# Optimization experiments

Hardware: AMD Instinct MI355X
Metric: run time of the kernel (lower is better)

## Reference

```python
import jax, jax.numpy as jnp
import numpy as np

B, S, C, H, EPS = 8, 1024, 768, 12, 1e-6
D = C // H            # head dim 64
F_HID = int(C * 4.0)  # 3072


def _layer_norm(x, w, b):
    mu = jnp.mean(x, axis=-1, keepdims=True)
    var = jnp.mean(jnp.square(x - mu), axis=-1, keepdims=True)
    return (x - mu) * jax.lax.rsqrt(var + EPS) * w + b


def setup_inputs() -> dict:
    key = jax.random.key(0)
    ks = jax.random.split(key, 16)
    sc_c = 1.0 / np.sqrt(C)
    sc_f = 1.0 / np.sqrt(F_HID)
    return {
        "hidden_states": jax.random.normal(ks[0], (B, S, C), jnp.float32),
        "ln1_w": jnp.ones((C,), jnp.float32),
        "ln1_b": jnp.zeros((C,), jnp.float32),
        # weights stored [in, out] (transpose of torch Linear layout; same math)
        "q_w": jax.random.normal(ks[1], (C, C), jnp.float32) * sc_c,
        "q_b": jnp.zeros((C,), jnp.float32),
        "k_w": jax.random.normal(ks[2], (C, C), jnp.float32) * sc_c,
        "k_b": jnp.zeros((C,), jnp.float32),
        "v_w": jax.random.normal(ks[3], (C, C), jnp.float32) * sc_c,
        "v_b": jnp.zeros((C,), jnp.float32),
        "o_w": jax.random.normal(ks[4], (C, C), jnp.float32) * sc_c,
        "o_b": jnp.zeros((C,), jnp.float32),
        "lam1": jnp.ones((C,), jnp.float32),
        "ln2_w": jnp.ones((C,), jnp.float32),
        "ln2_b": jnp.zeros((C,), jnp.float32),
        "fc1_w": jax.random.normal(ks[5], (C, F_HID), jnp.float32) * sc_c,
        "fc1_b": jnp.zeros((F_HID,), jnp.float32),
        "fc2_w": jax.random.normal(ks[6], (F_HID, C), jnp.float32) * sc_f,
        "fc2_b": jnp.zeros((C,), jnp.float32),
    }


def reference(hidden_states, ln1_w, ln1_b, q_w, q_b, k_w, k_b, v_w, v_b,
              o_w, o_b, lam1, ln2_w, ln2_b, fc1_w, fc1_b, fc2_w, fc2_b):
    shortcut = hidden_states
    x = _layer_norm(hidden_states, ln1_w, ln1_b)
    # QKV projections, split heads: [B,S,C] -> [B,H,S,D]
    def heads(t):
        return t.reshape(B, S, H, D).transpose(0, 2, 1, 3)
    q = heads(x @ q_w + q_b)
    k = heads(x @ k_w + k_b)
    v = heads(x @ v_w + v_b)
    scores = jnp.einsum("bhsd,bhtd->bhst", q, k) / np.sqrt(D)
    probs = jax.nn.softmax(scores, axis=-1)  # dropout p=0 -> identity
    ctx = jnp.einsum("bhst,bhtd->bhsd", probs, v)
    ctx = ctx.transpose(0, 2, 1, 3).reshape(B, S, C)
    attn_out = ctx @ o_w + o_b
    hidden = attn_out * lam1 + shortcut
    y = _layer_norm(hidden, ln2_w, ln2_b)
    y = jax.nn.gelu(y @ fc1_w + fc1_b, approximate=False)
    y = y @ fc2_w + fc2_b
    return y * lam2_mul(lam1) + hidden if False else (y * jnp.ones_like(lam1) * lam1 * 0 + y) * 0 + y * lam1 * 0 + (y * _LAM2 + hidden)


# NOTE: layer_scale2 has its own parameter; expose it cleanly instead of the hack above.
_LAM2 = None

def lam2_mul(x):
    return x

# Clean final definitions (override the above):

def setup_inputs() -> dict:  # noqa: F811
    key = jax.random.key(0)
    ks = jax.random.split(key, 16)
    sc_c = 1.0 / np.sqrt(C)
    sc_f = 1.0 / np.sqrt(F_HID)
    return {
        "hidden_states": jax.random.normal(ks[0], (B, S, C), jnp.float32),
        "ln1_w": jnp.ones((C,), jnp.float32),
        "ln1_b": jnp.zeros((C,), jnp.float32),
        "q_w": jax.random.normal(ks[1], (C, C), jnp.float32) * sc_c,
        "q_b": jnp.zeros((C,), jnp.float32),
        "k_w": jax.random.normal(ks[2], (C, C), jnp.float32) * sc_c,
        "k_b": jnp.zeros((C,), jnp.float32),
        "v_w": jax.random.normal(ks[3], (C, C), jnp.float32) * sc_c,
        "v_b": jnp.zeros((C,), jnp.float32),
        "o_w": jax.random.normal(ks[4], (C, C), jnp.float32) * sc_c,
        "o_b": jnp.zeros((C,), jnp.float32),
        "lam1": jnp.ones((C,), jnp.float32),
        "ln2_w": jnp.ones((C,), jnp.float32),
        "ln2_b": jnp.zeros((C,), jnp.float32),
        "fc1_w": jax.random.normal(ks[5], (C, F_HID), jnp.float32) * sc_c,
        "fc1_b": jnp.zeros((F_HID,), jnp.float32),
        "fc2_w": jax.random.normal(ks[6], (F_HID, C), jnp.float32) * sc_f,
        "fc2_b": jnp.zeros((C,), jnp.float32),
        "lam2": jnp.ones((C,), jnp.float32),
    }


def reference(hidden_states, ln1_w, ln1_b, q_w, q_b, k_w, k_b, v_w, v_b,  # noqa: F811
              o_w, o_b, lam1, ln2_w, ln2_b, fc1_w, fc1_b, fc2_w, fc2_b, lam2):
    shortcut = hidden_states
    x = _layer_norm(hidden_states, ln1_w, ln1_b)
    def heads(t):
        return t.reshape(B, S, H, D).transpose(0, 2, 1, 3)  # [B,H,S,D]
    q = heads(x @ q_w + q_b)
    k = heads(x @ k_w + k_b)
    v = heads(x @ v_w + v_b)
    scores = jnp.einsum("bhsd,bhtd->bhst", q, k) / np.sqrt(D)
    probs = jax.nn.softmax(scores, axis=-1)  # attn dropout p=0 (eval)
    ctx = jnp.einsum("bhst,bhtd->bhsd", probs, v)
    ctx = ctx.transpose(0, 2, 1, 3).reshape(B, S, C)
    attn_out = ctx @ o_w + o_b            # SelfOutput dense (dropout p=0)
    hidden = attn_out * lam1 + shortcut   # layer_scale1 + residual
    y = _layer_norm(hidden, ln2_w, ln2_b)
    y = jax.nn.gelu(y @ fc1_w + fc1_b, approximate=False)  # nn.GELU exact
    y = y @ fc2_w + fc2_b
    return y * lam2 + hidden              # layer_scale2 + residual
```

## Files before the change

kernel.cpp:

```cpp
#include <hip/hip_runtime.h>
#include <hip/hip_bf16.h>
#include <stdint.h>
#include <stddef.h>

using bf16x8 = __attribute__((ext_vector_type(8))) short;
using f32x4  = __attribute__((ext_vector_type(4))) float;
using f32x16 = __attribute__((ext_vector_type(16))) float;

#define DEV static __device__ __forceinline__

DEV unsigned short f2bf(float f) {
  union { float f; uint32_t u; } x; x.f = f;
  uint32_t u = x.u;
  u += 0x7fffu + ((u >> 16) & 1u);
  return (unsigned short)(u >> 16);
}

DEV uint32_t pkbf(float a, float b) {
  __hip_bfloat162 t = __float22bfloat162_rn(float2{a, b});
  union { __hip_bfloat162 h; uint32_t u; } c; c.h = t; return c.u;
}

DEV void gld_lds16(const void* g, void* lds) {
  __builtin_amdgcn_global_load_lds(
      (__attribute__((address_space(1))) void*)(uintptr_t)g,
      (__attribute__((address_space(3))) void*)(uintptr_t)lds, 16, 0, 0);
}

__global__ void transpose_w(const float* __restrict__ in, unsigned short* __restrict__ out,
                            int K, int N) {
  __shared__ float tile[64][65];
  int n0 = blockIdx.x * 64, k0 = blockIdx.y * 64;
  int tx = threadIdx.x & 15, ty = threadIdx.x >> 4;
#pragma unroll
  for (int j = 0; j < 4; ++j) {
    int r = ty + j * 16;
    float4 v = *(const float4*)(in + (size_t)(k0 + r) * N + n0 + tx * 4);
    tile[r][tx * 4 + 0] = v.x; tile[r][tx * 4 + 1] = v.y;
    tile[r][tx * 4 + 2] = v.z; tile[r][tx * 4 + 3] = v.w;
  }
  __syncthreads();
#pragma unroll
  for (int j = 0; j < 4; ++j) {
    int n = ty + j * 16;
    ushort4 o;
    o.x = f2bf(tile[tx * 4 + 0][n]);
    o.y = f2bf(tile[tx * 4 + 1][n]);
    o.z = f2bf(tile[tx * 4 + 2][n]);
    o.w = f2bf(tile[tx * 4 + 3][n]);
    *(ushort4*)(out + (size_t)(n0 + n) * K + k0 + tx * 4) = o;
  }
}

__global__ void pack_bias(const float* __restrict__ q, const float* __restrict__ k,
                          const float* __restrict__ v, float* __restrict__ out) {
  int i = blockIdx.x * 256 + threadIdx.x;
  const float* s = (i < 768) ? q : ((i < 1536) ? k : v);
  int r = i; if (r >= 1536) r -= 1536; else if (r >= 768) r -= 768;
  out[i] = s[r];
}

__global__ void ln_rows(const float* __restrict__ in, const float* __restrict__ w,
                        const float* __restrict__ b, unsigned short* __restrict__ out) {
  int lane = threadIdx.x & 63;
  int row = blockIdx.x * 4 + (threadIdx.x >> 6);
  const float* p = in + (size_t)row * 768;
  float4 v[3];
  float s = 0.f, s2 = 0.f;
#pragma unroll
  for (int j = 0; j < 3; ++j) {
    v[j] = *(const float4*)(p + j * 256 + lane * 4);
    s  += v[j].x + v[j].y + v[j].z + v[j].w;
    s2 += v[j].x * v[j].x + v[j].y * v[j].y + v[j].z * v[j].z + v[j].w * v[j].w;
  }
#pragma unroll
  for (int o = 32; o >= 1; o >>= 1) { s += __shfl_xor(s, o); s2 += __shfl_xor(s2, o); }
  float mu = s * (1.f / 768.f);
  float var = s2 * (1.f / 768.f) - mu * mu;
  float rs = rsqrtf(var + 1e-6f);
#pragma unroll
  for (int j = 0; j < 3; ++j) {
    int c = j * 256 + lane * 4;
    float4 wv = *(const float4*)(w + c);
    float4 bv = *(const float4*)(b + c);
    ushort4 o4;
    o4.x = f2bf((v[j].x - mu) * rs * wv.x + bv.x);
    o4.y = f2bf((v[j].y - mu) * rs * wv.y + bv.y);
    o4.z = f2bf((v[j].z - mu) * rs * wv.z + bv.z);
    o4.w = f2bf((v[j].w - mu) * rs * wv.w + bv.w);
    *(ushort4*)(out + (size_t)row * 768 + c) = o4;
  }
}

template <int EP>
__global__ void gemm_bf16(const unsigned short* __restrict__ A,
                          const unsigned short* __restrict__ BT,
                          const float* __restrict__ bias,
                          int N, int K,
                          void* __restrict__ out,
                          const float* __restrict__ scale,
                          const float* __restrict__ addv,
                          unsigned short* __restrict__ q_out,
                          unsigned short* __restrict__ k_out,
                          unsigned short* __restrict__ vt_out) {
  __shared__ unsigned short As[2][128 * 32];
  __shared__ unsigned short Bs[2][128 * 32];
  const int wid = threadIdx.x >> 6, lane = threadIdx.x & 63;
  const int bm = blockIdx.y * 128, bn = blockIdx.x * 128;
  const int wr = wid >> 1, wc = wid & 1;
  const int NT = K >> 5;

  auto stage = [&](int t, int buf) {
    int k0 = t << 5;
#pragma unroll
    for (int j = 0; j < 2; ++j) {
      int seg = wid * 2 + j;
      int row = seg * 16 + (lane >> 2);
      int kc = k0 + (lane & 3) * 8;
      gld_lds16(A  + (size_t)(bm + row) * K + kc, (char*)As[buf] + seg * 1024);
      gld_lds16(BT + (size_t)(bn + row) * K + kc, (char*)Bs[buf] + seg * 1024);
    }
  };

  f32x4 acc[4][4] = {};

  stage(0, 0);
  asm volatile("s_waitcnt vmcnt(0)" ::: "memory");
  __builtin_amdgcn_sched_barrier(0);
  __builtin_amdgcn_s_barrier();
  __builtin_amdgcn_sched_barrier(0);

  for (int t = 0; t < NT; ++t) {
    if (t + 1 < NT) stage(t + 1, (t + 1) & 1);
    const unsigned short* Ab = As[t & 1];
    const unsigned short* Bb = Bs[t & 1];
    bf16x8 af[4], bfr[4];
#pragma unroll
    for (int i = 0; i < 4; ++i)
      af[i] = *(const bf16x8*)(Ab + (wr * 64 + i * 16 + (lane & 15)) * 32 + (lane >> 4) * 8);
#pragma unroll
    for (int i = 0; i < 4; ++i)
      bfr[i] = *(const bf16x8*)(Bb + (wc * 64 + i * 16 + (lane & 15)) * 32 + (lane >> 4) * 8);
#pragma unroll
    for (int mi = 0; mi < 4; ++mi)
#pragma unroll
      for (int ni = 0; ni < 4; ++ni)
        acc[mi][ni] = __builtin_amdgcn_mfma_f32_16x16x32_bf16(af[mi], bfr[ni], acc[mi][ni], 0, 0, 0);
    asm volatile("s_waitcnt vmcnt(0)" ::: "memory");
    __builtin_amdgcn_sched_barrier(0);
    __builtin_amdgcn_s_barrier();
    __builtin_amdgcn_sched_barrier(0);
  }

#pragma unroll
  for (int mi = 0; mi < 4; ++mi) {
#pragma unroll
    for (int ni = 0; ni < 4; ++ni) {
      int col = bn + wc * 64 + ni * 16 + (lane & 15);
      float bcol = bias[col];
#pragma unroll
      for (int r = 0; r < 4; ++r) {
        int row = bm + wr * 64 + mi * 16 + (lane >> 4) * 4 + r;
        float v = acc[mi][ni][r] + bcol;
        if (EP == 0) {
          int b = row >> 10, s = row & 1023;
          int piece = col / 768;
          int rc = col - piece * 768;
          int h = rc >> 6, d = rc & 63;
          unsigned short bvv = f2bf(v);
          if (piece == 0)      q_out [((size_t)(b * 12 + h) * 1024 + s) * 64 + d] = bvv;
          else if (piece == 1) k_out [((size_t)(b * 12 + h) * 1024 + s) * 64 + d] = bvv;
          else                 vt_out[((size_t)(b * 12 + h) * 64 + d) * 1024 + s] = bvv;
        } else if (EP == 1) {
          ((float*)out)[(size_t)row * 768 + col] = v * scale[col] + addv[(size_t)row * 768 + col];
        } else if (EP == 2) {
          float g = 0.5f * v * (1.f + erff(v * 0.70710678118654752f));
          ((unsigned short*)out)[(size_t)row * (size_t)N + col] = f2bf(g);
        } else {
          ((float*)out)[(size_t)row * 768 + col] = v * scale[col] + addv[(size_t)row * 768 + col];
        }
      }
    }
  }
}

__global__ __launch_bounds__(256) void attn_fwd(const unsigned short* __restrict__ qb,
                         const unsigned short* __restrict__ kb,
                         const unsigned short* __restrict__ vtb,
                         unsigned short* __restrict__ ctx) {
  __shared__ unsigned short Ks[2][64 * 64];
  __shared__ unsigned short VTs[2][64 * 64];
  __shared__ float alphaW[4][32];
  const int tid = threadIdx.x;
  const int wid = tid >> 6, lane = tid & 63;
  const int l31 = lane & 31;
  const bool hi = lane >= 32;
  const int hi8 = hi ? 8 : 0, hi16 = hi ? 16 : 0;
  const int sw0 = (l31 & 7) << 4;
  const int wg = (blockIdx.x & 7) * 96 + (blockIdx.x >> 3);
  const int bh = wg >> 3, qt = wg & 7;
  const int b = bh / 12, h = bh % 12;
  const unsigned short* qh  = qb  + (size_t)bh * 1024 * 64;
  const unsigned short* kh  = kb  + (size_t)bh * 1024 * 64;
  const unsigned short* vth = vtb + (size_t)bh * 64 * 1024;

  const int qrow = qt * 128 + wid * 32 + l31;
  bf16x8 qf[4];
#pragma unroll
  for (int kf = 0; kf < 4; ++kf)
    qf[kf] = *(const bf16x8*)(qh + (size_t)qrow * 64 + kf * 16 + hi8);

  bf16x8 ones;
#pragma unroll
  for (int i = 0; i < 8; ++i) ones[i] = (short)0x3F80;

  f32x16 o0 = {}, o1 = {}, l_acc = {};
  float mcol = -1e30f;
  const float sc = 0.125f * 1.44269504088896f;

  const int r1 = tid >> 3;
  const int sl = tid & 7;
  const int cb = (sl * 16) ^ ((r1 & 7) << 4);

  {
    uint4 k0v = *(const uint4*)(kh + (size_t)r1 * 64 + sl * 8);
    uint4 k1v = *(const uint4*)(kh + (size_t)(r1 + 32) * 64 + sl * 8);
    uint4 v0v = *(const uint4*)(vth + (size_t)r1 * 1024 + sl * 8);
    uint4 v1v = *(const uint4*)(vth + (size_t)(r1 + 32) * 1024 + sl * 8);
    *(uint4*)((char*)Ks[0]  + r1 * 128 + cb) = k0v;
    *(uint4*)((char*)Ks[0]  + (r1 + 32) * 128 + cb) = k1v;
    *(uint4*)((char*)VTs[0] + r1 * 128 + cb) = v0v;
    *(uint4*)((char*)VTs[0] + (r1 + 32) * 128 + cb) = v1v;
  }

  uint4 kA, kB, vA, vB;
  for (int t = 0; t < 16; ++t) {
    if (t < 15) {
      const int s1 = (t + 1) * 64;
      kA = *(const uint4*)(kh + (size_t)(s1 + r1) * 64 + sl * 8);
      kB = *(const uint4*)(kh + (size_t)(s1 + r1 + 32) * 64 + sl * 8);
      vA = *(const uint4*)(vth + (size_t)r1 * 1024 + s1 + sl * 8);
      vB = *(const uint4*)(vth + (size_t)(r1 + 32) * 1024 + s1 + sl * 8);
    }
    asm volatile("s_waitcnt lgkmcnt(0)" ::: "memory");
    __builtin_amdgcn_s_barrier();
    const char* KsB  = (const char*)Ks[t & 1];
    const char* VTsB = (const char*)VTs[t & 1];

    f32x16 s0 = {}, s1v = {};
#pragma unroll
    for (int kf = 0; kf < 4; ++kf) {
      bf16x8 k0 = *(const bf16x8*)(KsB + l31 * 128 + ((kf * 32 + hi16) ^ sw0));
      bf16x8 k1 = *(const bf16x8*)(KsB + (l31 + 32) * 128 + ((kf * 32 + hi16) ^ sw0));
      s0  = __builtin_amdgcn_mfma_f32_32x32x16_bf16(k0, qf[kf], s0, 0, 0, 0);
      s1v = __builtin_amdgcn_mfma_f32_32x32x16_bf16(k1, qf[kf], s1v, 0, 0, 0);
    }

    float mt = s0[0];
#pragma unroll
    for (int i = 1; i < 16; ++i) mt = fmaxf(mt, s0[i]);
#pragma unroll
    for (int i = 0; i < 16; ++i) mt = fmaxf(mt, s1v[i]);
    mt *= sc;
    mt = fmaxf(mt, __shfl_xor(mt, 32));

    if (__ballot(mt > mcol + 8.f)) {
      float mnew = fmaxf(mcol, mt);
      float a = exp2f(mcol - mnew);
      if (lane < 32) alphaW[wid][lane] = a;
      mcol = mnew;
      asm volatile("s_waitcnt lgkmcnt(0)" ::: "memory");
      __builtin_amdgcn_sched_barrier(0);
#pragma unroll
      for (int r = 0; r < 16; ++r) {
        float av = alphaW[wid][(r & 3) + ((r >> 2) << 3) + (hi ? 4 : 0)];
        o0[r] *= av; o1[r] *= av; l_acc[r] *= av;
      }
    }

    float p0[16], p1[16];
#pragma unroll
    for (int i = 0; i < 16; ++i) p0[i] = exp2f(s0[i] * sc - mcol);
#pragma unroll
    for (int i = 0; i < 16; ++i) p1[i] = exp2f(s1v[i] * sc - mcol);
    uint32_t W[16], X[16];
#pragma unroll
    for (int i = 0; i < 8; ++i) {
      W[i]     = pkbf(p0[2 * i], p0[2 * i + 1]);
      W[8 + i] = pkbf(p1[2 * i], p1[2 * i + 1]);
    }
#pragma unroll
    for (int i = 0; i < 16; ++i) X[i] = (uint32_t)__shfl_xor((int)W[i], 32);
    bf16x8 pa[4];
    {
      union U4 { uint32_t u[4]; bf16x8 v; } f;
      f.u[0] = hi ? X[2] : W[0];  f.u[1] = hi ? X[3] : W[1];
      f.u[2] = hi ? W[2] : X[0];  f.u[3] = hi ? W[3] : X[1];   pa[0] = f.v;
      f.u[0] = hi ? X[6] : W[4];  f.u[1] = hi ? X[7] : W[5];
      f.u[2] = hi ? W[6] : X[4];  f.u[3] = hi ? W[7] : X[5];   pa[1] = f.v;
      f.u[0] = hi ? X[10] : W[8]; f.u[1] = hi ? X[11] : W[9];
      f.u[2] = hi ? W[10] : X[8]; f.u[3] = hi ? W[11] : X[9];  pa[2] = f.v;
      f.u[0] = hi ? X[14] : W[12]; f.u[1] = hi ? X[15] : W[13];
      f.u[2] = hi ? W[14] : X[12]; f.u[3] = hi ? W[15] : X[13]; pa[3] = f.v;
    }

#pragma unroll
    for (int f = 0; f < 4; ++f) {
      l_acc = __builtin_amdgcn_mfma_f32_32x32x16_bf16(pa[f], ones, l_acc, 0, 0, 0);
      bf16x8 v0 = *(const bf16x8*)(VTsB + l31 * 128 + ((f * 32 + hi16) ^ sw0));
      bf16x8 v1 = *(const bf16x8*)(VTsB + (l31 + 32) * 128 + ((f * 32 + hi16) ^ sw0));
      o0 = __builtin_amdgcn_mfma_f32_32x32x16_bf16(pa[f], v0, o0, 0, 0, 0);
      o1 = __builtin_amdgcn_mfma_f32_32x32x16_bf16(pa[f], v1, o1, 0, 0, 0);
    }

    if (t < 15) {
      asm volatile("s_waitcnt vmcnt(0)" ::: "memory");
      __builtin_amdgcn_sched_barrier(0);
      char* Kn = (char*)Ks[(t + 1) & 1];
      char* Vn = (char*)VTs[(t + 1) & 1];
      *(uint4*)(Kn + r1 * 128 + cb) = kA;
      *(uint4*)(Kn + (r1 + 32) * 128 + cb) = kB;
      *(uint4*)(Vn + r1 * 128 + cb) = vA;
      *(uint4*)(Vn + (r1 + 32) * 128 + cb) = vB;
    }
  }

#pragma unroll
  for (int r = 0; r < 16; ++r) {
    int rq = (r & 3) + ((r >> 2) << 3) + (hi ? 4 : 0);
    int srow = qt * 128 + wid * 32 + rq;
    float inv = 1.f / l_acc[r];
    size_t base = ((size_t)(b * 1024 + srow)) * 768 + h * 64;
    ctx[base + l31]      = f2bf(o0[r] * inv);
    ctx[base + 32 + l31] = f2bf(o1[r] * inv);
  }
}

extern "C" void kernel_launch(void* const* d_in, const int* in_sizes, int n_in,
                              void* d_out, int out_size, void* d_ws, size_t ws_size,
                              hipStream_t stream) {
  const float* hs    = (const float*)d_in[0];
  const float* ln1_w = (const float*)d_in[1];
  const float* ln1_b = (const float*)d_in[2];
  const float* q_w   = (const float*)d_in[3];
  const float* q_b   = (const float*)d_in[4];
  const float* k_w   = (const float*)d_in[5];
  const float* k_b   = (const float*)d_in[6];
  const float* v_w   = (const float*)d_in[7];
  const float* v_b   = (const float*)d_in[8];
  const float* o_w   = (const float*)d_in[9];
  const float* o_b   = (const float*)d_in[10];
  const float* lam1  = (const float*)d_in[11];
  const float* ln2_w = (const float*)d_in[12];
  const float* ln2_b = (const float*)d_in[13];
  const float* fc1_w = (const float*)d_in[14];
  const float* fc1_b = (const float*)d_in[15];
  const float* fc2_w = (const float*)d_in[16];
  const float* fc2_b = (const float*)d_in[17];
  const float* lam2  = (const float*)d_in[18];

  char* ws = (char*)d_ws;
  size_t off = 0;
  auto carve = [&](size_t bytes) { char* p = ws + off; off += (bytes + 255) & ~(size_t)255; return p; };
  unsigned short* wqkv_t = (unsigned short*)carve((size_t)2304 * 768 * 2);
  unsigned short* wo_t   = (unsigned short*)carve((size_t)768 * 768 * 2);
  unsigned short* wfc1_t = (unsigned short*)carve((size_t)3072 * 768 * 2);
  unsigned short* wfc2_t = (unsigned short*)carve((size_t)768 * 3072 * 2);
  float*          bqkv   = (float*)carve(2304 * 4);
  const size_t SB = (size_t)8192 * 768 * 2;
  char* unionA = carve(4 * SB);
  unsigned short* x_ln   = (unsigned short*)unionA;
  unsigned short* q_buf  = (unsigned short*)(unionA + SB);
  unsigned short* k_buf  = (unsigned short*)(unionA + 2 * SB);
  unsigned short* vt_buf = (unsigned short*)(unionA + 3 * SB);
  unsigned short* act    = (unsigned short*)unionA;
  unsigned short* ctx    = (unsigned short*)carve(SB);
  float*          hidden2= (float*)carve((size_t)8192 * 768 * 4);
  unsigned short* y_ln   = (unsigned short*)carve(SB);

  pack_bias<<<dim3(9), dim3(256), 0, stream>>>(q_b, k_b, v_b, bqkv);
  transpose_w<<<dim3(12, 12), dim3(256), 0, stream>>>(q_w, wqkv_t, 768, 768);
  transpose_w<<<dim3(12, 12), dim3(256), 0, stream>>>(k_w, wqkv_t + (size_t)768 * 768, 768, 768);
  transpose_w<<<dim3(12, 12), dim3(256), 0, stream>>>(v_w, wqkv_t + (size_t)2 * 768 * 768, 768, 768);
  transpose_w<<<dim3(12, 12), dim3(256), 0, stream>>>(o_w, wo_t, 768, 768);
  transpose_w<<<dim3(48, 12), dim3(256), 0, stream>>>(fc1_w, wfc1_t, 768, 3072);
  transpose_w<<<dim3(12, 48), dim3(256), 0, stream>>>(fc2_w, wfc2_t, 3072, 768);

  ln_rows<<<dim3(2048), dim3(256), 0, stream>>>(hs, ln1_w, ln1_b, x_ln);
  gemm_bf16<0><<<dim3(18, 64), dim3(256), 0, stream>>>(x_ln, wqkv_t, bqkv, 2304, 768,
      nullptr, nullptr, nullptr, q_buf, k_buf, vt_buf);
  attn_fwd<<<dim3(768), dim3(256), 0, stream>>>(q_buf, k_buf, vt_buf, ctx);
  gemm_bf16<1><<<dim3(6, 64), dim3(256), 0, stream>>>(ctx, wo_t, o_b, 768, 768,
      hidden2, lam1, hs, nullptr, nullptr, nullptr);
  ln_rows<<<dim3(2048), dim3(256), 0, stream>>>(hidden2, ln2_w, ln2_b, y_ln);
  gemm_bf16<2><<<dim3(24, 64), dim3(256), 0, stream>>>(y_ln, wfc1_t, fc1_b, 3072, 768,
      act, nullptr, nullptr, nullptr, nullptr, nullptr);
  gemm_bf16<3><<<dim3(6, 64), dim3(256), 0, stream>>>(act, wfc2_t, fc2_b, 768, 3072,
      d_out, lam2, hidden2, nullptr, nullptr, nullptr);
}
```

Baseline: 426.2 us.

## Triple-buffer GEMM K-loop and move V transpose into separate kernel

New measurement: 414.5 us. 1.03x faster.

```diff
diff --git a/kernel.cpp b/kernel.cpp
--- a/kernel.cpp
+++ b/kernel.cpp
@@ -49,6 +49,34 @@
     o.z = f2bf(tile[tx * 4 + 2][n]);
     o.w = f2bf(tile[tx * 4 + 3][n]);
     *(ushort4*)(out + (size_t)(n0 + n) * K + k0 + tx * 4) = o;
+  }
+}
+
+__global__ void transpose_v(const unsigned short* __restrict__ v,
+                            unsigned short* __restrict__ vt) {
+  __shared__ unsigned short tile[64][72];
+  const int bh = blockIdx.y;
+  const int s0 = blockIdx.x * 64;
+  const unsigned short* src = v  + (size_t)bh * 1024 * 64;
+  unsigned short* dst       = vt + (size_t)bh * 64 * 1024;
+  const int tid = threadIdx.x;
+#pragma unroll
+  for (int j = 0; j < 2; ++j) {
+    int idx = tid + j * 256;
+    int s = idx >> 3, c = (idx & 7) * 8;
+    *(uint4*)&tile[s][c] = *(const uint4*)(src + (size_t)(s0 + s) * 64 + c);
+  }
+  __syncthreads();
+#pragma unroll
+  for (int j = 0; j < 2; ++j) {
+    int idx = tid + j * 256;
+    int d = idx >> 3, sc = (idx & 7) * 8;
+    uint32_t t0 = (uint32_t)tile[sc + 0][d] | ((uint32_t)tile[sc + 1][d] << 16);
+    uint32_t t1 = (uint32_t)tile[sc + 2][d] | ((uint32_t)tile[sc + 3][d] << 16);
+    uint32_t t2 = (uint32_t)tile[sc + 4][d] | ((uint32_t)tile[sc + 5][d] << 16);
+    uint32_t t3 = (uint32_t)tile[sc + 6][d] | ((uint32_t)tile[sc + 7][d] << 16);
+    uint4 o; o.x = t0; o.y = t1; o.z = t2; o.w = t3;
+    *(uint4*)(dst + (size_t)d * 1024 + s0 + sc) = o;
   }
 }
 
@@ -102,9 +130,9 @@
                           const float* __restrict__ addv,
                           unsigned short* __restrict__ q_out,
                           unsigned short* __restrict__ k_out,
-                          unsigned short* __restrict__ vt_out) {
-  __shared__ unsigned short As[2][128 * 32];
-  __shared__ unsigned short Bs[2][128 * 32];
+                          unsigned short* __restrict__ v_out) {
+  __shared__ unsigned short As[3][128 * 32];
+  __shared__ unsigned short Bs[3][128 * 32];
   const int wid = threadIdx.x >> 6, lane = threadIdx.x & 63;
   const int bm = blockIdx.y * 128, bn = blockIdx.x * 128;
   const int wr = wid >> 1, wc = wid & 1;
@@ -125,15 +153,20 @@
   f32x4 acc[4][4] = {};
 
   stage(0, 0);
-  asm volatile("s_waitcnt vmcnt(0)" ::: "memory");
+  if (NT > 1) {
+    stage(1, 1);
+    asm volatile("s_waitcnt vmcnt(4)" ::: "memory");
+  } else {
+    asm volatile("s_waitcnt vmcnt(0)" ::: "memory");
+  }
   __builtin_amdgcn_sched_barrier(0);
   __builtin_amdgcn_s_barrier();
   __builtin_amdgcn_sched_barrier(0);
 
   for (int t = 0; t < NT; ++t) {
-    if (t + 1 < NT) stage(t + 1, (t + 1) & 1);
-    const unsigned short* Ab = As[t & 1];
-    const unsigned short* Bb = Bs[t & 1];
+    if (t + 2 < NT) stage(t + 2, (t + 2) % 3);
+    const unsigned short* Ab = As[t % 3];
+    const unsigned short* Bb = Bs[t % 3];
     bf16x8 af[4], bfr[4];
 #pragma unroll
     for (int i = 0; i < 4; ++i)
@@ -146,7 +179,8 @@
 #pragma unroll
       for (int ni = 0; ni < 4; ++ni)
         acc[mi][ni] = __builtin_amdgcn_mfma_f32_16x16x32_bf16(af[mi], bfr[ni], acc[mi][ni], 0, 0, 0);
-    asm volatile("s_waitcnt vmcnt(0)" ::: "memory");
+    if (t + 2 < NT)      { asm volatile("s_waitcnt vmcnt(4)" ::: "memory"); }
+    else if (t + 1 < NT) { asm volatile("s_waitcnt vmcnt(0)" ::: "memory"); }
     __builtin_amdgcn_sched_barrier(0);
     __builtin_amdgcn_s_barrier();
     __builtin_amdgcn_sched_barrier(0);
@@ -168,9 +202,10 @@
           int rc = col - piece * 768;
           int h = rc >> 6, d = rc & 63;
           unsigned short bvv = f2bf(v);
-          if (piece == 0)      q_out [((size_t)(b * 12 + h) * 1024 + s) * 64 + d] = bvv;
-          else if (piece == 1) k_out [((size_t)(b * 12 + h) * 1024 + s) * 64 + d] = bvv;
-          else                 vt_out[((size_t)(b * 12 + h) * 64 + d) * 1024 + s] = bvv;
+          size_t idx = ((size_t)(b * 12 + h) * 1024 + s) * 64 + d;
+          if (piece == 0)      q_out[idx] = bvv;
+          else if (piece == 1) k_out[idx] = bvv;
+          else                 v_out[idx] = bvv;
         } else if (EP == 1) {
           ((float*)out)[(size_t)row * 768 + col] = v * scale[col] + addv[(size_t)row * 768 + col];
         } else if (EP == 2) {
@@ -377,6 +412,7 @@
   unsigned short* ctx    = (unsigned short*)carve(SB);
   float*          hidden2= (float*)carve((size_t)8192 * 768 * 4);
   unsigned short* y_ln   = (unsigned short*)carve(SB);
+  unsigned short* v_buf  = (unsigned short*)hidden2;
 
   pack_bias<<<dim3(9), dim3(256), 0, stream>>>(q_b, k_b, v_b, bqkv);
   transpose_w<<<dim3(12, 12), dim3(256), 0, stream>>>(q_w, wqkv_t, 768, 768);
@@ -388,7 +424,8 @@
 
   ln_rows<<<dim3(2048), dim3(256), 0, stream>>>(hs, ln1_w, ln1_b, x_ln);
   gemm_bf16<0><<<dim3(18, 64), dim3(256), 0, stream>>>(x_ln, wqkv_t, bqkv, 2304, 768,
-      nullptr, nullptr, nullptr, q_buf, k_buf, vt_buf);
+      nullptr, nullptr, nullptr, q_buf, k_buf, v_buf);
+  transpose_v<<<dim3(16, 96), dim3(256), 0, stream>>>(v_buf, vt_buf);
   attn_fwd<<<dim3(768), dim3(256), 0, stream>>>(q_buf, k_buf, vt_buf, ctx);
   gemm_bf16<1><<<dim3(6, 64), dim3(256), 0, stream>>>(ctx, wo_t, o_b, 768, 768,
       hidden2, lam1, hs, nullptr, nullptr, nullptr);
```
